# Performance work log

Measured on AMD Instinct MI355X. Metric: run time of the kernel, lower is better.

## Reference

```python
import jax, jax.numpy as jnp
import numpy as np

NUM_GROUPS = 32
EPS = 1e-5
SLOPE = 0.1  # LeakyReLU negative slope

B, N, M = 4, 65536, 16384
C_IN, C_OUT = 512, 256


def _unary(x, W, b, gamma, beta):
    # Linear -> GroupNorm(32) over channel dim per point -> LeakyReLU(0.1)
    h = jnp.einsum('bnc,cd->bnd', x, W) + b          # (B, N, C_out)
    Bb, Nn, C = h.shape
    hg = h.reshape(Bb, Nn, NUM_GROUPS, C // NUM_GROUPS)
    mu = hg.mean(axis=-1, keepdims=True)
    var = hg.var(axis=-1, keepdims=True)
    hn = ((hg - mu) * jax.lax.rsqrt(var + EPS)).reshape(Bb, Nn, C)
    hn = hn * gamma + beta
    return jnp.where(hn >= 0, hn, SLOPE * hn)


def setup_inputs() -> dict:
    key = jax.random.key(0)
    ks = jax.random.split(key, 12)
    query = jax.random.normal(ks[0], (B, N, C_OUT), dtype=jnp.float32)
    support = jax.random.normal(ks[1], (B, M, C_IN), dtype=jnp.float32)
    upsample_indices = jax.random.randint(ks[2], (B, N, 1), 0, M, dtype=jnp.int32)
    s1 = 1.0 / np.sqrt(C_IN)
    s2 = 1.0 / np.sqrt(C_OUT)
    return {
        'query': query,
        'support': support,
        'upsample_indices': upsample_indices,
        'W1': jax.random.normal(ks[3], (C_IN, C_OUT), dtype=jnp.float32) * s1,
        'b1': jnp.zeros((C_OUT,), jnp.float32),
        'g1': jnp.ones((C_OUT,), jnp.float32),
        'be1': jnp.zeros((C_OUT,), jnp.float32),
        'W2': jax.random.normal(ks[4], (C_OUT, C_OUT), dtype=jnp.float32) * s2,
        'b2': jnp.zeros((C_OUT,), jnp.float32),
        'g2': jnp.ones((C_OUT,), jnp.float32),
        'be2': jnp.zeros((C_OUT,), jnp.float32),
        'W3': jax.random.normal(ks[5], (C_OUT, C_OUT), dtype=jnp.float32) * s2,
        'b3': jnp.zeros((C_OUT,), jnp.float32),
        'g3': jnp.ones((C_OUT,), jnp.float32),
        'be3': jnp.zeros((C_OUT,), jnp.float32),
    }


def reference(query, support, upsample_indices, W1, b1, g1, be1, W2, b2, g2, be2, W3, b3, g3, be3):
    # knn_gather with K=1 then squeeze: latent[b, n] = support[b, idx[b, n, 0]]
    batch_ids = jnp.arange(support.shape[0])[:, None]          # (B, 1)
    latent = support[batch_ids, upsample_indices[:, :, 0]]      # (B, N, C_IN)
    h = _unary(latent, W1, b1, g1, be1)
    h = _unary(h, W2, b2, g2, be2)
    return _unary(h + query, W3, b3, g3, be3)
```

## Files before the change

kernel.cpp:

```cpp
#include <hip/hip_runtime.h>

typedef __attribute__((ext_vector_type(8))) _Float16 half8;
typedef __attribute__((ext_vector_type(4))) _Float16 half4;
typedef __attribute__((ext_vector_type(4))) float f32x4;

static constexpr int NB   = 4;
static constexpr int NQ   = 65536;
static constexpr int MS   = 16384;
static constexpr int CIN  = 512;
static constexpr int COUT = 256;
static constexpr int TR   = 64;
static constexpr float EPSV = 1e-5f;
static constexpr float SLP  = 0.1f;

__global__ void prep_split(const float* __restrict__ W,
                           _Float16* __restrict__ hi, _Float16* __restrict__ lo,
                           int K, int D) {
  int i = blockIdx.x * 256 + threadIdx.x;
  if (i >= K * D) return;
  int k = i / D, d = i - k * D;
  float v = W[i];
  _Float16 h = (_Float16)v;
  _Float16 l = (_Float16)(v - (float)h);
  hi[(size_t)d * K + k] = h;
  lo[(size_t)d * K + k] = l;
}

__device__ __forceinline__ int swz(int row, int colByte) {
  return row * 512 + (colByte ^ ((row & 15) << 4));
}

__global__ void __launch_bounds__(256, 2)
fused_main(const float* __restrict__ query, const float* __restrict__ support,
           const int* __restrict__ uidx,
           const float* __restrict__ b1, const float* __restrict__ g1, const float* __restrict__ be1,
           const float* __restrict__ b2, const float* __restrict__ g2, const float* __restrict__ be2,
           const float* __restrict__ b3, const float* __restrict__ g3, const float* __restrict__ be3,
           const _Float16* __restrict__ w1h, const _Float16* __restrict__ w1l,
           const _Float16* __restrict__ w2h, const _Float16* __restrict__ w2l,
           const _Float16* __restrict__ w3h, const _Float16* __restrict__ w3l,
           float* __restrict__ out)
{
  __shared__ _Float16 sHi[TR * 256];
  __shared__ _Float16 sLo[TR * 256];
  __shared__ int sIdx[TR];
  char* dhi = (char*)sHi;
  char* dlo = (char*)sLo;

  const int tid  = threadIdx.x;
  const int lane = tid & 63;
  const int wid  = tid >> 6;
  const int c0   = wid * 64;
  const int r0   = blockIdx.x * TR;
  const int bb   = r0 >> 16;

  if (tid < TR) sIdx[tid] = uidx[r0 + tid];
  __syncthreads();

  const int arow  = lane & 15;
  const int kslot = (lane >> 4) * 8;

  f32x4 acc[4][4];

  #pragma unroll
  for (int nt = 0; nt < 4; ++nt) {
    float bc = b1[c0 + nt * 16 + arow];
    #pragma unroll
    for (int mt = 0; mt < 4; ++mt) acc[mt][nt] = (f32x4){bc, bc, bc, bc};
  }

  #pragma unroll 1
  for (int ck = 0; ck < 2; ++ck) {
    {
      int grow = tid >> 2;
      int gcol = (tid & 3) * 64;
      const float* src = support + (size_t)bb * MS * CIN
                       + (size_t)sIdx[grow] * CIN + ck * 256 + gcol;
      #pragma unroll
      for (int i = 0; i < 16; ++i) {
        f32x4 v = *(const f32x4*)(src + i * 4);
        half4 h, l;
        #pragma unroll
        for (int j = 0; j < 4; ++j) {
          _Float16 hh = (_Float16)v[j];
          h[j] = hh;
          l[j] = (_Float16)(v[j] - (float)hh);
        }
        int cb = (gcol + i * 4) * 2;
        *(half4*)(dhi + swz(grow, cb)) = h;
        *(half4*)(dlo + swz(grow, cb)) = l;
      }
    }
    __syncthreads();

    #pragma unroll 2
    for (int ks = 0; ks < 8; ++ks) {
      int kk = ks * 32 + kslot;
      half8 Ah[4], Al[4];
      #pragma unroll
      for (int mt = 0; mt < 4; ++mt) {
        Ah[mt] = *(const half8*)(dhi + swz(mt * 16 + arow, kk * 2));
        Al[mt] = *(const half8*)(dlo + swz(mt * 16 + arow, kk * 2));
      }
      #pragma unroll
      for (int nt = 0; nt < 4; ++nt) {
        size_t wo = (size_t)(c0 + nt * 16 + arow) * 512 + ck * 256 + kk;
        half8 Bh = *(const half8*)(w1h + wo);
        half8 Bl = *(const half8*)(w1l + wo);
        #pragma unroll
        for (int mt = 0; mt < 4; ++mt) {
          acc[mt][nt] = __builtin_amdgcn_mfma_f32_16x16x32_f16(Ah[mt], Bh, acc[mt][nt], 0, 0, 0);
          acc[mt][nt] = __builtin_amdgcn_mfma_f32_16x16x32_f16(Al[mt], Bh, acc[mt][nt], 0, 0, 0);
          acc[mt][nt] = __builtin_amdgcn_mfma_f32_16x16x32_f16(Ah[mt], Bl, acc[mt][nt], 0, 0, 0);
        }
      }
    }
    __syncthreads();
  }

  #pragma unroll
  for (int nt = 0; nt < 4; ++nt) {
    int c = c0 + nt * 16 + arow;
    float gm = g1[c], bt = be1[c];
    #pragma unroll
    for (int mt = 0; mt < 4; ++mt) {
      f32x4 v = acc[mt][nt];
      #pragma unroll
      for (int j = 0; j < 4; ++j) {
        float x = v[j];
        float s = x, q = x * x;
        s += __shfl_xor(s, 1); q += __shfl_xor(q, 1);
        s += __shfl_xor(s, 2); q += __shfl_xor(q, 2);
        s += __shfl_xor(s, 4); q += __shfl_xor(q, 4);
        float mu  = s * 0.125f;
        float var = fmaf(q, 0.125f, -mu * mu);
        float inv = rsqrtf(var + EPSV);
        float hn  = fmaf((x - mu) * inv, gm, bt);
        hn = hn >= 0.f ? hn : SLP * hn;
        int row = mt * 16 + (lane >> 4) * 4 + j;
        _Float16 hh = (_Float16)hn;
        *(_Float16*)(dhi + swz(row, c * 2)) = hh;
        *(_Float16*)(dlo + swz(row, c * 2)) = (_Float16)(hn - (float)hh);
      }
    }
  }
  __syncthreads();

  #pragma unroll
  for (int nt = 0; nt < 4; ++nt) {
    float bc = b2[c0 + nt * 16 + arow];
    #pragma unroll
    for (int mt = 0; mt < 4; ++mt) acc[mt][nt] = (f32x4){bc, bc, bc, bc};
  }
  #pragma unroll 2
  for (int ks = 0; ks < 8; ++ks) {
    int kk = ks * 32 + kslot;
    half8 Ah[4], Al[4];
    #pragma unroll
    for (int mt = 0; mt < 4; ++mt) {
      Ah[mt] = *(const half8*)(dhi + swz(mt * 16 + arow, kk * 2));
      Al[mt] = *(const half8*)(dlo + swz(mt * 16 + arow, kk * 2));
    }
    #pragma unroll
    for (int nt = 0; nt < 4; ++nt) {
      size_t wo = (size_t)(c0 + nt * 16 + arow) * 256 + kk;
      half8 Bh = *(const half8*)(w2h + wo);
      half8 Bl = *(const half8*)(w2l + wo);
      #pragma unroll
      for (int mt = 0; mt < 4; ++mt) {
        acc[mt][nt] = __builtin_amdgcn_mfma_f32_16x16x32_f16(Ah[mt], Bh, acc[mt][nt], 0, 0, 0);
        acc[mt][nt] = __builtin_amdgcn_mfma_f32_16x16x32_f16(Al[mt], Bh, acc[mt][nt], 0, 0, 0);
        acc[mt][nt] = __builtin_amdgcn_mfma_f32_16x16x32_f16(Ah[mt], Bl, acc[mt][nt], 0, 0, 0);
      }
    }
  }
  __syncthreads();

  #pragma unroll
  for (int nt = 0; nt < 4; ++nt) {
    int c = c0 + nt * 16 + arow;
    float gm = g2[c], bt = be2[c];
    #pragma unroll
    for (int mt = 0; mt < 4; ++mt) {
      f32x4 v = acc[mt][nt];
      #pragma unroll
      for (int j = 0; j < 4; ++j) {
        float x = v[j];
        float s = x, q = x * x;
        s += __shfl_xor(s, 1); q += __shfl_xor(q, 1);
        s += __shfl_xor(s, 2); q += __shfl_xor(q, 2);
        s += __shfl_xor(s, 4); q += __shfl_xor(q, 4);
        float mu  = s * 0.125f;
        float var = fmaf(q, 0.125f, -mu * mu);
        float inv = rsqrtf(var + EPSV);
        float hn  = fmaf((x - mu) * inv, gm, bt);
        hn = hn >= 0.f ? hn : SLP * hn;
        int row = mt * 16 + (lane >> 4) * 4 + j;
        float x3 = hn + query[(size_t)(r0 + row) * COUT + c];
        _Float16 hh = (_Float16)x3;
        *(_Float16*)(dhi + swz(row, c * 2)) = hh;
        *(_Float16*)(dlo + swz(row, c * 2)) = (_Float16)(x3 - (float)hh);
      }
    }
  }
  __syncthreads();

  #pragma unroll
  for (int nt = 0; nt < 4; ++nt) {
    float bc = b3[c0 + nt * 16 + arow];
    #pragma unroll
    for (int mt = 0; mt < 4; ++mt) acc[mt][nt] = (f32x4){bc, bc, bc, bc};
  }
  #pragma unroll 2
  for (int ks = 0; ks < 8; ++ks) {
    int kk = ks * 32 + kslot;
    half8 Ah[4], Al[4];
    #pragma unroll
    for (int mt = 0; mt < 4; ++mt) {
      Ah[mt] = *(const half8*)(dhi + swz(mt * 16 + arow, kk * 2));
      Al[mt] = *(const half8*)(dlo + swz(mt * 16 + arow, kk * 2));
    }
    #pragma unroll
    for (int nt = 0; nt < 4; ++nt) {
      size_t wo = (size_t)(c0 + nt * 16 + arow) * 256 + kk;
      half8 Bh = *(const half8*)(w3h + wo);
      half8 Bl = *(const half8*)(w3l + wo);
      #pragma unroll
      for (int mt = 0; mt < 4; ++mt) {
        acc[mt][nt] = __builtin_amdgcn_mfma_f32_16x16x32_f16(Ah[mt], Bh, acc[mt][nt], 0, 0, 0);
        acc[mt][nt] = __builtin_amdgcn_mfma_f32_16x16x32_f16(Al[mt], Bh, acc[mt][nt], 0, 0, 0);
        acc[mt][nt] = __builtin_amdgcn_mfma_f32_16x16x32_f16(Ah[mt], Bl, acc[mt][nt], 0, 0, 0);
      }
    }
  }

  #pragma unroll
  for (int nt = 0; nt < 4; ++nt) {
    int c = c0 + nt * 16 + arow;
    float gm = g3[c], bt = be3[c];
    #pragma unroll
    for (int mt = 0; mt < 4; ++mt) {
      f32x4 v = acc[mt][nt];
      #pragma unroll
      for (int j = 0; j < 4; ++j) {
        float x = v[j];
        float s = x, q = x * x;
        s += __shfl_xor(s, 1); q += __shfl_xor(q, 1);
        s += __shfl_xor(s, 2); q += __shfl_xor(q, 2);
        s += __shfl_xor(s, 4); q += __shfl_xor(q, 4);
        float mu  = s * 0.125f;
        float var = fmaf(q, 0.125f, -mu * mu);
        float inv = rsqrtf(var + EPSV);
        float hn  = fmaf((x - mu) * inv, gm, bt);
        hn = hn >= 0.f ? hn : SLP * hn;
        int row = mt * 16 + (lane >> 4) * 4 + j;
        out[(size_t)(r0 + row) * COUT + c] = hn;
      }
    }
  }
}

extern "C" void kernel_launch(void* const* d_in, const int* in_sizes, int n_in,
                              void* d_out, int out_size, void* d_ws, size_t ws_size,
                              hipStream_t stream) {
  const float* query   = (const float*)d_in[0];
  const float* support = (const float*)d_in[1];
  const int*   uidx    = (const int*)d_in[2];
  const float* W1  = (const float*)d_in[3];
  const float* b1  = (const float*)d_in[4];
  const float* g1  = (const float*)d_in[5];
  const float* be1 = (const float*)d_in[6];
  const float* W2  = (const float*)d_in[7];
  const float* b2  = (const float*)d_in[8];
  const float* g2  = (const float*)d_in[9];
  const float* be2 = (const float*)d_in[10];
  const float* W3  = (const float*)d_in[11];
  const float* b3  = (const float*)d_in[12];
  const float* g3  = (const float*)d_in[13];
  const float* be3 = (const float*)d_in[14];
  float* out = (float*)d_out;

  char* ws = (char*)d_ws;
  _Float16* w1h = (_Float16*)ws;
  _Float16* w1l = w1h + (size_t)CIN * COUT;
  _Float16* w2h = w1l + (size_t)CIN * COUT;
  _Float16* w2l = w2h + (size_t)COUT * COUT;
  _Float16* w3h = w2l + (size_t)COUT * COUT;
  _Float16* w3l = w3h + (size_t)COUT * COUT;

  prep_split<<<(CIN * COUT + 255) / 256, 256, 0, stream>>>(W1, w1h, w1l, CIN, COUT);
  prep_split<<<(COUT * COUT + 255) / 256, 256, 0, stream>>>(W2, w2h, w2l, COUT, COUT);
  prep_split<<<(COUT * COUT + 255) / 256, 256, 0, stream>>>(W3, w3h, w3l, COUT, COUT);

  fused_main<<<(NB * NQ) / TR, 256, 0, stream>>>(
      query, support, uidx,
      b1, g1, be1, b2, g2, be2, b3, g3, be3,
      w1h, w1l, w2h, w2l, w3h, w3l, out);
}
```

Before: 1.162 ms.

## Split each 64-row tile across 8 waves to halve per-wave accumulators

Doubles the block to 512 threads, with waves split two ways over rows (32 rows each) and four ways over output channels. Each wave now holds half the accumulator registers, which aims at more resident waves per CU to hide gather and global weight-load latency. The gather loop is re-split over 512 threads and now writes 8-wide half vectors to LDS. The cost is that each wave reloads the same B weight fragments from global memory twice as often per tile, and the MFMA-to-load ratio per wave goes down.

```diff
diff --git a/kernel.cpp b/kernel.cpp
--- a/kernel.cpp
+++ b/kernel.cpp
@@ -30,7 +30,7 @@
   return row * 512 + (colByte ^ ((row & 15) << 4));
 }
 
-__global__ void __launch_bounds__(256, 2)
+__global__ void __launch_bounds__(512, 4)
 fused_main(const float* __restrict__ query, const float* __restrict__ support,
            const int* __restrict__ uidx,
            const float* __restrict__ b1, const float* __restrict__ g1, const float* __restrict__ be1,
@@ -50,7 +50,8 @@
   const int tid  = threadIdx.x;
   const int lane = tid & 63;
   const int wid  = tid >> 6;
-  const int c0   = wid * 64;
+  const int m0   = (wid >> 2) * 32;
+  const int c0   = (wid & 3) * 64;
   const int r0   = blockIdx.x * TR;
   const int bb   = r0 >> 16;
 
@@ -60,35 +61,37 @@
   const int arow  = lane & 15;
   const int kslot = (lane >> 4) * 8;
 
-  f32x4 acc[4][4];
+  f32x4 acc[2][4];
 
   #pragma unroll
   for (int nt = 0; nt < 4; ++nt) {
     float bc = b1[c0 + nt * 16 + arow];
     #pragma unroll
-    for (int mt = 0; mt < 4; ++mt) acc[mt][nt] = (f32x4){bc, bc, bc, bc};
+    for (int mt = 0; mt < 2; ++mt) acc[mt][nt] = (f32x4){bc, bc, bc, bc};
   }
 
   #pragma unroll 1
   for (int ck = 0; ck < 2; ++ck) {
     {
-      int grow = tid >> 2;
-      int gcol = (tid & 3) * 64;
+      int grow = tid >> 3;
+      int gcol = (tid & 7) * 32;
       const float* src = support + (size_t)bb * MS * CIN
                        + (size_t)sIdx[grow] * CIN + ck * 256 + gcol;
       #pragma unroll
-      for (int i = 0; i < 16; ++i) {
-        f32x4 v = *(const f32x4*)(src + i * 4);
-        half4 h, l;
+      for (int i = 0; i < 4; ++i) {
+        f32x4 va = *(const f32x4*)(src + i * 8);
+        f32x4 vb = *(const f32x4*)(src + i * 8 + 4);
+        half8 h, l;
         #pragma unroll
         for (int j = 0; j < 4; ++j) {
-          _Float16 hh = (_Float16)v[j];
-          h[j] = hh;
-          l[j] = (_Float16)(v[j] - (float)hh);
+          _Float16 ha = (_Float16)va[j];
+          _Float16 hb = (_Float16)vb[j];
+          h[j]     = ha;           l[j]     = (_Float16)(va[j] - (float)ha);
+          h[j + 4] = hb;           l[j + 4] = (_Float16)(vb[j] - (float)hb);
         }
-        int cb = (gcol + i * 4) * 2;
-        *(half4*)(dhi + swz(grow, cb)) = h;
-        *(half4*)(dlo + swz(grow, cb)) = l;
+        int cb = (gcol + i * 8) * 2;
+        *(half8*)(dhi + swz(grow, cb)) = h;
+        *(half8*)(dlo + swz(grow, cb)) = l;
       }
     }
     __syncthreads();
@@ -96,11 +99,11 @@
     #pragma unroll 2
     for (int ks = 0; ks < 8; ++ks) {
       int kk = ks * 32 + kslot;
-      half8 Ah[4], Al[4];
-      #pragma unroll
-      for (int mt = 0; mt < 4; ++mt) {
-        Ah[mt] = *(const half8*)(dhi + swz(mt * 16 + arow, kk * 2));
-        Al[mt] = *(const half8*)(dlo + swz(mt * 16 + arow, kk * 2));
+      half8 Ah[2], Al[2];
+      #pragma unroll
+      for (int mt = 0; mt < 2; ++mt) {
+        Ah[mt] = *(const half8*)(dhi + swz(m0 + mt * 16 + arow, kk * 2));
+        Al[mt] = *(const half8*)(dlo + swz(m0 + mt * 16 + arow, kk * 2));
       }
       #pragma unroll
       for (int nt = 0; nt < 4; ++nt) {
@@ -108,7 +111,7 @@
         half8 Bh = *(const half8*)(w1h + wo);
         half8 Bl = *(const half8*)(w1l + wo);
         #pragma unroll
-        for (int mt = 0; mt < 4; ++mt) {
+        for (int mt = 0; mt < 2; ++mt) {
           acc[mt][nt] = __builtin_amdgcn_mfma_f32_16x16x32_f16(Ah[mt], Bh, acc[mt][nt], 0, 0, 0);
           acc[mt][nt] = __builtin_amdgcn_mfma_f32_16x16x32_f16(Al[mt], Bh, acc[mt][nt], 0, 0, 0);
           acc[mt][nt] = __builtin_amdgcn_mfma_f32_16x16x32_f16(Ah[mt], Bl, acc[mt][nt], 0, 0, 0);
@@ -123,7 +126,7 @@
     int c = c0 + nt * 16 + arow;
     float gm = g1[c], bt = be1[c];
     #pragma unroll
-    for (int mt = 0; mt < 4; ++mt) {
+    for (int mt = 0; mt < 2; ++mt) {
       f32x4 v = acc[mt][nt];
       #pragma unroll
       for (int j = 0; j < 4; ++j) {
@@ -137,7 +140,7 @@
         float inv = rsqrtf(var + EPSV);
         float hn  = fmaf((x - mu) * inv, gm, bt);
         hn = hn >= 0.f ? hn : SLP * hn;
-        int row = mt * 16 + (lane >> 4) * 4 + j;
+        int row = m0 + mt * 16 + (lane >> 4) * 4 + j;
         _Float16 hh = (_Float16)hn;
         *(_Float16*)(dhi + swz(row, c * 2)) = hh;
         *(_Float16*)(dlo + swz(row, c * 2)) = (_Float16)(hn - (float)hh);
@@ -150,16 +153,16 @@
   for (int nt = 0; nt < 4; ++nt) {
     float bc = b2[c0 + nt * 16 + arow];
     #pragma unroll
-    for (int mt = 0; mt < 4; ++mt) acc[mt][nt] = (f32x4){bc, bc, bc, bc};
+    for (int mt = 0; mt < 2; ++mt) acc[mt][nt] = (f32x4){bc, bc, bc, bc};
   }
   #pragma unroll 2
   for (int ks = 0; ks < 8; ++ks) {
     int kk = ks * 32 + kslot;
-    half8 Ah[4], Al[4];
-    #pragma unroll
-    for (int mt = 0; mt < 4; ++mt) {
-      Ah[mt] = *(const half8*)(dhi + swz(mt * 16 + arow, kk * 2));
-      Al[mt] = *(const half8*)(dlo + swz(mt * 16 + arow, kk * 2));
+    half8 Ah[2], Al[2];
+    #pragma unroll
+    for (int mt = 0; mt < 2; ++mt) {
+      Ah[mt] = *(const half8*)(dhi + swz(m0 + mt * 16 + arow, kk * 2));
+      Al[mt] = *(const half8*)(dlo + swz(m0 + mt * 16 + arow, kk * 2));
     }
     #pragma unroll
     for (int nt = 0; nt < 4; ++nt) {
@@ -167,7 +170,7 @@
       half8 Bh = *(const half8*)(w2h + wo);
       half8 Bl = *(const half8*)(w2l + wo);
       #pragma unroll
-      for (int mt = 0; mt < 4; ++mt) {
+      for (int mt = 0; mt < 2; ++mt) {
         acc[mt][nt] = __builtin_amdgcn_mfma_f32_16x16x32_f16(Ah[mt], Bh, acc[mt][nt], 0, 0, 0);
         acc[mt][nt] = __builtin_amdgcn_mfma_f32_16x16x32_f16(Al[mt], Bh, acc[mt][nt], 0, 0, 0);
         acc[mt][nt] = __builtin_amdgcn_mfma_f32_16x16x32_f16(Ah[mt], Bl, acc[mt][nt], 0, 0, 0);
@@ -181,7 +184,7 @@
     int c = c0 + nt * 16 + arow;
     float gm = g2[c], bt = be2[c];
     #pragma unroll
-    for (int mt = 0; mt < 4; ++mt) {
+    for (int mt = 0; mt < 2; ++mt) {
       f32x4 v = acc[mt][nt];
       #pragma unroll
       for (int j = 0; j < 4; ++j) {
@@ -195,7 +198,7 @@
         float inv = rsqrtf(var + EPSV);
         float hn  = fmaf((x - mu) * inv, gm, bt);
         hn = hn >= 0.f ? hn : SLP * hn;
-        int row = mt * 16 + (lane >> 4) * 4 + j;
+        int row = m0 + mt * 16 + (lane >> 4) * 4 + j;
         float x3 = hn + query[(size_t)(r0 + row) * COUT + c];
         _Float16 hh = (_Float16)x3;
         *(_Float16*)(dhi + swz(row, c * 2)) = hh;
@@ -209,16 +212,16 @@
   for (int nt = 0; nt < 4; ++nt) {
     float bc = b3[c0 + nt * 16 + arow];
     #pragma unroll
-    for (int mt = 0; mt < 4; ++mt) acc[mt][nt] = (f32x4){bc, bc, bc, bc};
+    for (int mt = 0; mt < 2; ++mt) acc[mt][nt] = (f32x4){bc, bc, bc, bc};
   }
   #pragma unroll 2
   for (int ks = 0; ks < 8; ++ks) {
     int kk = ks * 32 + kslot;
-    half8 Ah[4], Al[4];
-    #pragma unroll
-    for (int mt = 0; mt < 4; ++mt) {
-      Ah[mt] = *(const half8*)(dhi + swz(mt * 16 + arow, kk * 2));
-      Al[mt] = *(const half8*)(dlo + swz(mt * 16 + arow, kk * 2));
+    half8 Ah[2], Al[2];
+    #pragma unroll
+    for (int mt = 0; mt < 2; ++mt) {
+      Ah[mt] = *(const half8*)(dhi + swz(m0 + mt * 16 + arow, kk * 2));
+      Al[mt] = *(const half8*)(dlo + swz(m0 + mt * 16 + arow, kk * 2));
     }
     #pragma unroll
     for (int nt = 0; nt < 4; ++nt) {
@@ -226,7 +229,7 @@
       half8 Bh = *(const half8*)(w3h + wo);
       half8 Bl = *(const half8*)(w3l + wo);
       #pragma unroll
-      for (int mt = 0; mt < 4; ++mt) {
+      for (int mt = 0; mt < 2; ++mt) {
         acc[mt][nt] = __builtin_amdgcn_mfma_f32_16x16x32_f16(Ah[mt], Bh, acc[mt][nt], 0, 0, 0);
         acc[mt][nt] = __builtin_amdgcn_mfma_f32_16x16x32_f16(Al[mt], Bh, acc[mt][nt], 0, 0, 0);
         acc[mt][nt] = __builtin_amdgcn_mfma_f32_16x16x32_f16(Ah[mt], Bl, acc[mt][nt], 0, 0, 0);
@@ -239,7 +242,7 @@
     int c = c0 + nt * 16 + arow;
     float gm = g3[c], bt = be3[c];
     #pragma unroll
-    for (int mt = 0; mt < 4; ++mt) {
+    for (int mt = 0; mt < 2; ++mt) {
       f32x4 v = acc[mt][nt];
       #pragma unroll
       for (int j = 0; j < 4; ++j) {
@@ -253,7 +256,7 @@
         float inv = rsqrtf(var + EPSV);
         float hn  = fmaf((x - mu) * inv, gm, bt);
         hn = hn >= 0.f ? hn : SLP * hn;
-        int row = mt * 16 + (lane >> 4) * 4 + j;
+        int row = m0 + mt * 16 + (lane >> 4) * 4 + j;
         out[(size_t)(r0 + row) * COUT + c] = hn;
       }
     }
@@ -292,7 +295,7 @@
   prep_split<<<(COUT * COUT + 255) / 256, 256, 0, stream>>>(W2, w2h, w2l, COUT, COUT);
   prep_split<<<(COUT * COUT + 255) / 256, 256, 0, stream>>>(W3, w3h, w3l, COUT, COUT);
 
-  fused_main<<<(NB * NQ) / TR, 256, 0, stream>>>(
+  fused_main<<<(NB * NQ) / TR, 512, 0, stream>>>(
       query, support, uidx,
       b1, g1, be1, b2, g2, be2, b3, g3, be3,
       w1h, w1l, w2h, w2l, w3h, w3l, out);
```

Measured after the change: 1.546 ms. +33.1%, slower.
